# Kernel tuning notes

Hardware: AMD Instinct MI355X
Metric: run time of the kernel (lower is better)

The kernel has to match this reference:

```python
import jax, jax.numpy as jnp
import numpy as np

TEMPERATURE = 0.1
INF = 1e8
SIGMA = (5.0, 1.0)
LABEL_TYPE = ("cont", "cat")
CAT_SIM = (0.0, 0.5)
ALPHA = (1.0, 1.0)
N, D = 4096, 128


def _label_weights(y, label_type, sigma, cat_sim):
    # y: [2N] label values; returns row-normalized RBF weight matrix [2N, 2N]
    gamma = 1.0 / (2.0 * sigma ** 2)
    d2 = (y[:, None] - y[None, :]) ** 2
    w = jnp.exp(-gamma * d2)
    if label_type == "cat":
        # rbf == 1 exactly iff labels equal; others snapped to cat_similarity
        w = jnp.where(w == 1.0, 1.0, cat_sim)
    n2 = w.shape[0]
    w = w * (1.0 - jnp.eye(n2, dtype=w.dtype))
    w = w / jnp.sum(w, axis=1, keepdims=True)
    return w


def setup_inputs() -> dict:
    key = jax.random.key(0)
    k1, k2, k3, k4 = jax.random.split(key, 4)
    z_i = jax.random.normal(k1, (N, D), dtype=jnp.float32)
    z_j = jax.random.normal(k2, (N, D), dtype=jnp.float32)
    cont = jax.random.normal(k3, (N,), dtype=jnp.float32) * 10.0  # e.g. age
    cat = jax.random.randint(k4, (N,), 0, 3).astype(jnp.float32)   # e.g. class id
    labels = jnp.stack([cont, cat], axis=1)  # [N, 2]
    return {"z_i": z_i, "z_j": z_j, "labels": labels}


def reference(z_i, z_j, labels):
    n = z_i.shape[0]
    zi = z_i / jnp.linalg.norm(z_i, axis=-1, keepdims=True)
    zj = z_j / jnp.linalg.norm(z_j, axis=-1, keepdims=True)
    eye = INF * jnp.eye(n, dtype=zi.dtype)
    sim_zii = zi @ zi.T / TEMPERATURE - eye
    sim_zjj = zj @ zj.T / TEMPERATURE - eye
    sim_zij = zi @ zj.T / TEMPERATURE
    sim_Z = jnp.concatenate(
        [jnp.concatenate([sim_zii, sim_zij], axis=1),
         jnp.concatenate([sim_zij.T, sim_zjj], axis=1)], axis=0)  # [2N, 2N]
    log_sim_Z = jax.nn.log_softmax(sim_Z, axis=1)
    loss = jnp.zeros((), dtype=sim_Z.dtype)
    for i, (lt, s, cs, a) in enumerate(zip(LABEL_TYPE, SIGMA, CAT_SIM, ALPHA)):
        y = jnp.tile(labels[:, i], 2)  # [2N] == repeat(2,1).flatten()
        w = _label_weights(y, lt, s, cs)
        loss = loss + (-1.0 / n) * jnp.sum(w * log_sim_Z) * a
    return loss
```

## Files before the change

### kernel.cpp

```cpp
#include <hip/hip_runtime.h>
#include <hip/hip_bf16.h>
#include <math.h>

#define NP 4096
#define DD 128
#define N2 8192
#define TINV 10.0f
#define SHIFT 10.0f
#define C1 14.4269504f
#define NGL2 -0.0288539004f

typedef __attribute__((ext_vector_type(8))) short bf16x8;
typedef __attribute__((ext_vector_type(4))) float f32x4;
typedef __attribute__((ext_vector_type(4))) int i32x4;

__device__ __forceinline__ float bf2f(short s) {
  return __uint_as_float(((unsigned)(unsigned short)s) << 16);
}

#define GLDS(g, l)                                                                   \
  __builtin_amdgcn_global_load_lds((__attribute__((address_space(1))) const void*)(g), \
                                   (__attribute__((address_space(3))) void*)(l), 16, 0, 0)

__device__ __forceinline__ float dpp_red16(float x) {
  x += __int_as_float(__builtin_amdgcn_update_dpp(0, __float_as_int(x), 0x101, 0xF, 0xF, true));
  x += __int_as_float(__builtin_amdgcn_update_dpp(0, __float_as_int(x), 0x102, 0xF, 0xF, true));
  x += __int_as_float(__builtin_amdgcn_update_dpp(0, __float_as_int(x), 0x104, 0xF, 0xF, true));
  x += __int_as_float(__builtin_amdgcn_update_dpp(0, __float_as_int(x), 0x108, 0xF, 0xF, true));
  return x;
}

__global__ __launch_bounds__(256) void kprep(const float* __restrict__ zi,
                                             const float* __restrict__ zj,
                                             const float* __restrict__ labels,
                                             __hip_bfloat16* __restrict__ Z,
                                             float4* __restrict__ rowinfo,
                                             double* __restrict__ accd,
                                             unsigned int* __restrict__ cnt,
                                             float* __restrict__ zsc) {
  int w = threadIdx.x >> 6, lane = threadIdx.x & 63;
  if (blockIdx.x < 2048) {
    int a = blockIdx.x * 4 + w;
    const float* src = (a < NP) ? (zi + (size_t)a * DD) : (zj + (size_t)(a - NP) * DD);
    float2 v = *(const float2*)(src + lane * 2);
    float ss = v.x * v.x + v.y * v.y;
#pragma unroll
    for (int m = 1; m < 64; m <<= 1) ss += __shfl_xor(ss, m);
    float rn = rsqrtf(ss);
    __hip_bfloat162 o;
    o.x = __float2bfloat16(v.x * rn);
    o.y = __float2bfloat16(v.y * rn);
    *(__hip_bfloat162*)(Z + (size_t)a * DD + lane * 2) = o;
  } else {
    int a = blockIdx.x - 2048;
    if (a == 0) {
      if (threadIdx.x == 0) { *accd = 0.0; cnt[0] = 0u; }
      for (int q = threadIdx.x; q < 384; q += 256) zsc[q] = 0.f;
    }
    float ca = labels[a * 2 + 0], ga = labels[a * 2 + 1];
    float s1 = 0.f, c2 = 0.f;
    for (int m = threadIdx.x; m < NP; m += 256) {
      float2 lm = *(const float2*)(labels + m * 2);
      float dy = ca - lm.x;
      s1 += __builtin_amdgcn_exp2f(dy * dy * NGL2);
      c2 += (ga == lm.y) ? 1.f : 0.f;
    }
#pragma unroll
    for (int m = 1; m < 64; m <<= 1) {
      s1 += __shfl_xor(s1, m);
      c2 += __shfl_xor(c2, m);
    }
    __shared__ float sh[8];
    if (lane == 0) { sh[w] = s1; sh[4 + w] = c2; }
    __syncthreads();
    if (threadIdx.x == 0) {
      s1 = sh[0] + sh[1] + sh[2] + sh[3];
      c2 = sh[4] + sh[5] + sh[6] + sh[7];
      float rs1 = 2.f * s1 - 1.f;
      float rs2 = (float)NP + c2 - 1.f;
      float4 ri = make_float4(ca, TINV / rs1, ga, TINV / rs2);
      rowinfo[a] = ri;
      rowinfo[a + NP] = ri;
    }
  }
}

__global__ __launch_bounds__(512, 4) void kmain(const __hip_bfloat16* __restrict__ Zp,
                                                const float4* __restrict__ rowinfo,
                                                const float* __restrict__ labels,
                                                float2* __restrict__ part,
                                                float* __restrict__ zsc) {
  __shared__ char lds[2 * 128 * 256 + 4 * 512 * 4];

  int id = (blockIdx.x & 7) * 268 + (blockIdx.x >> 3);
  const int t = threadIdx.x;
  const int lane = t & 63, w = t >> 6;

  if (id >= 2080) {
    int b = id - 2080;
    int c = t & 127, rgrp = t >> 7;
    int r0 = b * 128 + rgrp * 32;
    float s0 = 0.f, s1 = 0.f, s2 = 0.f;
    for (int k = 0; k < 32; ++k) {
      int r = r0 + k;
      float zf = bf2f(((const short*)Zp)[(size_t)r * DD + c]);
      float g = labels[(r & (NP - 1)) * 2 + 1];
      s0 += (g == 0.f) ? zf : 0.f;
      s1 += (g == 1.f) ? zf : 0.f;
      s2 += (g == 2.f) ? zf : 0.f;
    }
    float* sh = (float*)lds;
    sh[(rgrp * 3 + 0) * 128 + c] = s0;
    sh[(rgrp * 3 + 1) * 128 + c] = s1;
    sh[(rgrp * 3 + 2) * 128 + c] = s2;
    __syncthreads();
    if (t < 384) {
      int cls = t >> 7, cc = t & 127;
      float v = sh[(0 * 3 + cls) * 128 + cc] + sh[(1 * 3 + cls) * 128 + cc] +
                sh[(2 * 3 + cls) * 128 + cc] + sh[(3 * 3 + cls) * 128 + cc];
      atomicAdd(&zsc[cls * 128 + cc], v);
    }
    return;
  }

  char* ldsA = lds;
  char* ldsB = lds + 128 * 256;
  float* lacc = (float*)(lds + 2 * 128 * 256);
  int tb = id;
  int I = (int)((129.0f - sqrtf(16641.0f - 8.0f * (float)tb)) * 0.5f);
  while (I * (129 - I) / 2 > tb) --I;
  while ((I + 1) * (128 - I) / 2 <= tb) ++I;
  int J = I + (tb - I * (129 - I) / 2);
  const bool diag = (I == J);
  const int row0 = I * 128, col0 = J * 128;
  const char* gZ = (const char*)Zp;
  const char* ldsBp = diag ? ldsA : ldsB;

  const int wr = w >> 2, wc = w & 3;
  const int lrow = lane & 15, lgrp = lane >> 4;

#pragma unroll
  for (int i = 0; i < 4; ++i) {
    int chunk = t + i * 512;
    int r = chunk >> 4;
    int bc = (chunk & 15) << 4;
    int srcc = bc ^ ((r & 7) << 4);
    int uoff = ((t & ~63) + i * 512) * 16;
    GLDS(gZ + (size_t)(row0 + r) * 256 + srcc, ldsA + uoff);
  }
  if (!diag) {
#pragma unroll
    for (int i = 0; i < 4; ++i) {
      int chunk = t + i * 512;
      int r = chunk >> 4;
      int bc = (chunk & 15) << 4;
      int srcc = bc ^ ((r & 7) << 4);
      int uoff = ((t & ~63) + i * 512) * 16;
      GLDS(gZ + (size_t)(col0 + r) * 256 + srcc, ldsB + uoff);
    }
  }
  __syncthreads();

  f32x4 acc[4][2] = {};
#pragma unroll
  for (int kk = 0; kk < 4; ++kk) {
    int bcol = kk * 64 + (lgrp << 4);
    bf16x8 af[4], bfv[2];
#pragma unroll
    for (int mi = 0; mi < 4; ++mi) {
      int r = wr * 64 + mi * 16 + lrow;
      af[mi] = *(const bf16x8*)(ldsA + r * 256 + (bcol ^ ((r & 7) << 4)));
    }
#pragma unroll
    for (int ni = 0; ni < 2; ++ni) {
      int r = wc * 32 + ni * 16 + lrow;
      bfv[ni] = *(const bf16x8*)(ldsBp + r * 256 + (bcol ^ ((r & 7) << 4)));
    }
#pragma unroll
    for (int mi = 0; mi < 4; ++mi)
#pragma unroll
      for (int ni = 0; ni < 2; ++ni)
        acc[mi][ni] = __builtin_amdgcn_mfma_f32_16x16x32_bf16(af[mi], bfv[ni], acc[mi][ni], 0, 0, 0);
  }

  float2 rbv[2];
#pragma unroll
  for (int ni = 0; ni < 2; ++ni)
    rbv[ni] = *(const float2*)&rowinfo[col0 + wc * 32 + ni * 16 + lrow];

  if (!diag) {
    float ec[2] = {0.f, 0.f}, pc[2] = {0.f, 0.f};
#pragma unroll
    for (int mi = 0; mi < 4; ++mi) {
      int a0 = row0 + wr * 64 + mi * 16 + lgrp * 4;
#pragma unroll
      for (int j = 0; j < 4; ++j) {
        float2 ri = *(const float2*)&rowinfo[a0 + j];
        float es = 0.f, pa = 0.f;
#pragma unroll
        for (int ni = 0; ni < 2; ++ni) {
          float v = acc[mi][ni][j];
          float e = __builtin_amdgcn_exp2f(fmaf(v, C1, -C1));
          float dy = ri.x - rbv[ni].x;
          float wu = __builtin_amdgcn_exp2f(dy * dy * NGL2);
          es += e;
          ec[ni] += e;
          pa = fmaf(wu, v, pa);
          pc[ni] = fmaf(wu, v, pc[ni]);
        }
        es = dpp_red16(es);
        float wsum = dpp_red16(pa * ri.y);
        if (lrow == 0) {
          int idx = wr * 64 + mi * 16 + lgrp * 4 + j;
          lacc[wc * 512 + 2 * idx] = es;
          lacc[wc * 512 + 2 * idx + 1] = wsum;
        }
      }
    }
#pragma unroll
    for (int ni = 0; ni < 2; ++ni) {
      float wcol = pc[ni] * rbv[ni].y;
      float e2 = ec[ni] + __shfl_xor(ec[ni], 16);
      e2 += __shfl_xor(e2, 32);
      float w2 = wcol + __shfl_xor(wcol, 16);
      w2 += __shfl_xor(w2, 32);
      if (lane < 16) {
        int idx = 128 + wc * 32 + ni * 16 + lane;
        lacc[wr * 512 + 2 * idx] = e2;
        lacc[wr * 512 + 2 * idx + 1] = w2;
      }
    }
  } else {
#pragma unroll
    for (int mi = 0; mi < 4; ++mi) {
      int a0 = row0 + wr * 64 + mi * 16 + lgrp * 4;
#pragma unroll
      for (int j = 0; j < 4; ++j) {
        int a = a0 + j;
        float2 ri = *(const float2*)&rowinfo[a0 + j];
        float es = 0.f, pa = 0.f;
#pragma unroll
        for (int ni = 0; ni < 2; ++ni) {
          float v = acc[mi][ni][j];
          float nd = (a != col0 + wc * 32 + ni * 16 + lrow) ? 1.f : 0.f;
          float e = __builtin_amdgcn_exp2f(fmaf(v, C1, -C1)) * nd;
          float dy = ri.x - rbv[ni].x;
          float wu = __builtin_amdgcn_exp2f(dy * dy * NGL2) * nd;
          es += e;
          pa = fmaf(wu, v, pa);
        }
        es = dpp_red16(es);
        float wsum = dpp_red16(pa * ri.y);
        if (lrow == 0) {
          int idx = wr * 64 + mi * 16 + lgrp * 4 + j;
          lacc[wc * 512 + 2 * idx] = es;
          lacc[wc * 512 + 2 * idx + 1] = wsum;
        }
      }
    }
    if (w < 2 && lane < 32) {
#pragma unroll
      for (int i = 0; i < 8; ++i) lacc[w * 512 + 256 + lane * 8 + i] = 0.f;
    }
  }

  __syncthreads();
  if (t < 256) {
    float2 p0 = ((float2*)lacc)[t];
    float2 p1 = ((float2*)lacc)[256 + t];
    float2 o;
    if (t < 128) {
      float2 p2 = ((float2*)lacc)[512 + t];
      float2 p3 = ((float2*)lacc)[768 + t];
      o.x = (p0.x + p1.x) + (p2.x + p3.x);
      o.y = (p0.y + p1.y) + (p2.y + p3.y);
    } else {
      o.x = p0.x + p1.x;
      o.y = p0.y + p1.y;
    }
    part[(size_t)tb * 256 + t] = o;
  }
}

__global__ __launch_bounds__(512) void kreduce(const float2* __restrict__ part,
                                               const __hip_bfloat16* __restrict__ Z,
                                               const float4* __restrict__ rowinfo,
                                               const float* __restrict__ zsc,
                                               double* __restrict__ accd,
                                               unsigned int* __restrict__ cnt,
                                               float* __restrict__ out) {
  int T = blockIdx.x;
  int t = threadIdx.x;
  int r = t & 127, q = t >> 7;
  float es = 0.f, ws = 0.f;
  int tb0 = T * (129 - T) / 2;
  for (int k = q; k < 64 - T; k += 4) {
    float2 v = part[(size_t)(tb0 + k) * 256 + r];
    es += v.x;
    ws += v.y;
  }
  for (int I = q; I < T; I += 4) {
    float2 v = part[(size_t)(I * (129 - I) / 2 + T - I) * 256 + 128 + r];
    es += v.x;
    ws += v.y;
  }
  __shared__ float sess[512], swss[512];
  sess[q * 128 + r] = es;
  swss[q * 128 + r] = ws;
  __syncthreads();

  double val = 0.0;
  if (t < 128) {
    es = sess[t] + sess[128 + t] + sess[256 + t] + sess[384 + t];
    ws = swss[t] + swss[128 + t] + swss[256 + t] + swss[384 + t];
    int a = T * 128 + t;
    float4 ri = rowinfo[a];
    int cls = (int)ri.z;
    const float* zc = zsc + cls * DD;
    float d1 = 0.f, d2 = 0.f;
    const __hip_bfloat16* zrow = Z + (size_t)a * DD;
#pragma unroll
    for (int k = 0; k < 16; ++k) {
      bf16x8 zv = *(const bf16x8*)(zrow + k * 8);
#pragma unroll
      for (int e = 0; e < 8; ++e) {
        int col = k * 8 + e;
        float zf = bf2f(zv[e]);
        float tot = zsc[col] + zsc[128 + col] + zsc[256 + col];
        d1 = fmaf(zf, tot, d1);
        d2 = fmaf(zf, zc[col], d2);
      }
    }
    ws += (0.5f * (d1 - 1.0f) + 0.5f * (d2 - 1.0f)) * ri.w;
    val = (double)ws - 2.0 * (double)(SHIFT + __logf(es));
  }
#pragma unroll
  for (int m = 1; m < 64; m <<= 1) val += __shfl_xor(val, m);
  __shared__ double shd[8];
  if ((t & 63) == 0) shd[t >> 6] = val;
  __syncthreads();
  if (t == 0) {
    double bsum = shd[0] + shd[1] + shd[2] + shd[3] + shd[4] + shd[5] + shd[6] + shd[7];
    atomicAdd(accd, bsum);
    __threadfence();
    unsigned int old = atomicAdd(cnt, 1u);
    if (old == 63u) {
      double tot = atomicAdd(accd, 0.0);
      out[0] = (float)(-tot / (double)NP);
    }
  }
}

extern "C" void kernel_launch(void* const* d_in, const int* in_sizes, int n_in,
                              void* d_out, int out_size, void* d_ws, size_t ws_size,
                              hipStream_t stream) {
  const float* zi = (const float*)d_in[0];
  const float* zj = (const float*)d_in[1];
  const float* labels = (const float*)d_in[2];
  float* out = (float*)d_out;
  char* ws = (char*)d_ws;

  float4* rowinfo = (float4*)ws;
  double* accd = (double*)(ws + 128 * 1024);
  unsigned int* cnt = (unsigned int*)(ws + 128 * 1024 + 8);
  float* zsc = (float*)(ws + 132 * 1024);
  __hip_bfloat16* Z = (__hip_bfloat16*)(ws + 256 * 1024);
  float2* part = (float2*)(ws + 256 * 1024 + 2 * 1024 * 1024);

  kprep<<<6144, 256, 0, stream>>>(zi, zj, labels, Z, rowinfo, accd, cnt, zsc);
  kmain<<<2144, 512, 0, stream>>>(Z, rowinfo, labels, part, zsc);
  kreduce<<<64, 512, 0, stream>>>(part, Z, rowinfo, zsc, accd, cnt, out);
}
```

Baseline: 59.09 us.

## Make kmain persistent and prefetch the next tile during the epilogue

Replaces the 2144-block grid with 512 persistent blocks. Each block walks a strided list of tile IDs, and the zsc class-sum work is folded into the same loop. After the MFMA loop and a barrier, the next tile's global-to-LDS loads are issued before the exp/weight epilogue runs, so load latency overlaps the epilogue. This reduces block launch and first-load stalls, but the persistent blocks may load-balance less evenly and rely on barriers to order the LDS DMA.

Measured after the change: 87.73 us. 48.5% more time.

```diff
diff --git a/kernel.cpp b/kernel.cpp
--- a/kernel.cpp
+++ b/kernel.cpp
@@ -91,64 +91,27 @@
                                                 float2* __restrict__ part,
                                                 float* __restrict__ zsc) {
   __shared__ char lds[2 * 128 * 256 + 4 * 512 * 4];
-
-  int id = (blockIdx.x & 7) * 268 + (blockIdx.x >> 3);
-  const int t = threadIdx.x;
-  const int lane = t & 63, w = t >> 6;
-
-  if (id >= 2080) {
-    int b = id - 2080;
-    int c = t & 127, rgrp = t >> 7;
-    int r0 = b * 128 + rgrp * 32;
-    float s0 = 0.f, s1 = 0.f, s2 = 0.f;
-    for (int k = 0; k < 32; ++k) {
-      int r = r0 + k;
-      float zf = bf2f(((const short*)Zp)[(size_t)r * DD + c]);
-      float g = labels[(r & (NP - 1)) * 2 + 1];
-      s0 += (g == 0.f) ? zf : 0.f;
-      s1 += (g == 1.f) ? zf : 0.f;
-      s2 += (g == 2.f) ? zf : 0.f;
-    }
-    float* sh = (float*)lds;
-    sh[(rgrp * 3 + 0) * 128 + c] = s0;
-    sh[(rgrp * 3 + 1) * 128 + c] = s1;
-    sh[(rgrp * 3 + 2) * 128 + c] = s2;
-    __syncthreads();
-    if (t < 384) {
-      int cls = t >> 7, cc = t & 127;
-      float v = sh[(0 * 3 + cls) * 128 + cc] + sh[(1 * 3 + cls) * 128 + cc] +
-                sh[(2 * 3 + cls) * 128 + cc] + sh[(3 * 3 + cls) * 128 + cc];
-      atomicAdd(&zsc[cls * 128 + cc], v);
-    }
-    return;
-  }
-
   char* ldsA = lds;
   char* ldsB = lds + 128 * 256;
   float* lacc = (float*)(lds + 2 * 128 * 256);
-  int tb = id;
-  int I = (int)((129.0f - sqrtf(16641.0f - 8.0f * (float)tb)) * 0.5f);
-  while (I * (129 - I) / 2 > tb) --I;
-  while ((I + 1) * (128 - I) / 2 <= tb) ++I;
-  int J = I + (tb - I * (129 - I) / 2);
-  const bool diag = (I == J);
-  const int row0 = I * 128, col0 = J * 128;
-  const char* gZ = (const char*)Zp;
-  const char* ldsBp = diag ? ldsA : ldsB;
-
+
+  const int t = threadIdx.x;
+  const int lane = t & 63, w = t >> 6;
   const int wr = w >> 2, wc = w & 3;
   const int lrow = lane & 15, lgrp = lane >> 4;
-
-#pragma unroll
-  for (int i = 0; i < 4; ++i) {
-    int chunk = t + i * 512;
-    int r = chunk >> 4;
-    int bc = (chunk & 15) << 4;
-    int srcc = bc ^ ((r & 7) << 4);
-    int uoff = ((t & ~63) + i * 512) * 16;
-    GLDS(gZ + (size_t)(row0 + r) * 256 + srcc, ldsA + uoff);
-  }
-  if (!diag) {
+  const char* gZ = (const char*)Zp;
+
+  const int x = blockIdx.x & 7, l = blockIdx.x >> 3;
+  const int idbase = x * 268, idend = idbase + 268;
+
+  auto decode = [](int tb, int& I, int& J) {
+    int i0 = (int)((129.0f - sqrtf(16641.0f - 8.0f * (float)tb)) * 0.5f);
+    while (i0 * (129 - i0) / 2 > tb) --i0;
+    while ((i0 + 1) * (128 - i0) / 2 <= tb) ++i0;
+    I = i0;
+    J = i0 + (tb - i0 * (129 - i0) / 2);
+  };
+  auto stage = [&](int row0, int col0, bool diag) {
 #pragma unroll
     for (int i = 0; i < 4; ++i) {
       int chunk = t + i * 512;
@@ -156,129 +119,199 @@
       int bc = (chunk & 15) << 4;
       int srcc = bc ^ ((r & 7) << 4);
       int uoff = ((t & ~63) + i * 512) * 16;
-      GLDS(gZ + (size_t)(col0 + r) * 256 + srcc, ldsB + uoff);
+      GLDS(gZ + (size_t)(row0 + r) * 256 + srcc, ldsA + uoff);
+    }
+    if (!diag) {
+#pragma unroll
+      for (int i = 0; i < 4; ++i) {
+        int chunk = t + i * 512;
+        int r = chunk >> 4;
+        int bc = (chunk & 15) << 4;
+        int srcc = bc ^ ((r & 7) << 4);
+        int uoff = ((t & ~63) + i * 512) * 16;
+        GLDS(gZ + (size_t)(col0 + r) * 256 + srcc, ldsB + uoff);
+      }
+    }
+  };
+
+  int curI = 0, curJ = 0;
+  {
+    int id0 = idbase + l;
+    if (id0 < 2080) {
+      decode(id0, curI, curJ);
+      stage(curI * 128, curJ * 128, curI == curJ);
     }
   }
   __syncthreads();
 
-  f32x4 acc[4][2] = {};
-#pragma unroll
-  for (int kk = 0; kk < 4; ++kk) {
-    int bcol = kk * 64 + (lgrp << 4);
-    bf16x8 af[4], bfv[2];
-#pragma unroll
-    for (int mi = 0; mi < 4; ++mi) {
-      int r = wr * 64 + mi * 16 + lrow;
-      af[mi] = *(const bf16x8*)(ldsA + r * 256 + (bcol ^ ((r & 7) << 4)));
-    }
-#pragma unroll
-    for (int ni = 0; ni < 2; ++ni) {
-      int r = wc * 32 + ni * 16 + lrow;
-      bfv[ni] = *(const bf16x8*)(ldsBp + r * 256 + (bcol ^ ((r & 7) << 4)));
-    }
-#pragma unroll
-    for (int mi = 0; mi < 4; ++mi)
-#pragma unroll
-      for (int ni = 0; ni < 2; ++ni)
-        acc[mi][ni] = __builtin_amdgcn_mfma_f32_16x16x32_bf16(af[mi], bfv[ni], acc[mi][ni], 0, 0, 0);
-  }
-
-  float2 rbv[2];
-#pragma unroll
-  for (int ni = 0; ni < 2; ++ni)
-    rbv[ni] = *(const float2*)&rowinfo[col0 + wc * 32 + ni * 16 + lrow];
-
-  if (!diag) {
-    float ec[2] = {0.f, 0.f}, pc[2] = {0.f, 0.f};
-#pragma unroll
-    for (int mi = 0; mi < 4; ++mi) {
-      int a0 = row0 + wr * 64 + mi * 16 + lgrp * 4;
-#pragma unroll
-      for (int j = 0; j < 4; ++j) {
-        float2 ri = *(const float2*)&rowinfo[a0 + j];
-        float es = 0.f, pa = 0.f;
-#pragma unroll
-        for (int ni = 0; ni < 2; ++ni) {
-          float v = acc[mi][ni][j];
-          float e = __builtin_amdgcn_exp2f(fmaf(v, C1, -C1));
-          float dy = ri.x - rbv[ni].x;
-          float wu = __builtin_amdgcn_exp2f(dy * dy * NGL2);
-          es += e;
-          ec[ni] += e;
-          pa = fmaf(wu, v, pa);
-          pc[ni] = fmaf(wu, v, pc[ni]);
+  for (int k = 0; ; ++k) {
+    int id = idbase + l + 64 * k;
+    if (id >= idend) break;
+
+    if (id >= 2080) {
+      __syncthreads();
+      int b = id - 2080;
+      int c = t & 127, rgrp = t >> 7;
+      int r0 = b * 128 + rgrp * 32;
+      float s0 = 0.f, s1 = 0.f, s2 = 0.f;
+      for (int kk = 0; kk < 32; ++kk) {
+        int r = r0 + kk;
+        float zf = bf2f(((const short*)Zp)[(size_t)r * DD + c]);
+        float g = labels[(r & (NP - 1)) * 2 + 1];
+        s0 += (g == 0.f) ? zf : 0.f;
+        s1 += (g == 1.f) ? zf : 0.f;
+        s2 += (g == 2.f) ? zf : 0.f;
+      }
+      float* sh = (float*)lds;
+      sh[(rgrp * 3 + 0) * 128 + c] = s0;
+      sh[(rgrp * 3 + 1) * 128 + c] = s1;
+      sh[(rgrp * 3 + 2) * 128 + c] = s2;
+      __syncthreads();
+      if (t < 384) {
+        int cls = t >> 7, cc = t & 127;
+        float v = sh[(0 * 3 + cls) * 128 + cc] + sh[(1 * 3 + cls) * 128 + cc] +
+                  sh[(2 * 3 + cls) * 128 + cc] + sh[(3 * 3 + cls) * 128 + cc];
+        atomicAdd(&zsc[cls * 128 + cc], v);
+      }
+      continue;
+    }
+
+    const int row0 = curI * 128, col0 = curJ * 128;
+    const bool diag = (curI == curJ);
+    const char* ldsBp = diag ? ldsA : ldsB;
+
+    f32x4 acc[4][2] = {};
+#pragma unroll
+    for (int kk = 0; kk < 4; ++kk) {
+      int bcol = kk * 64 + (lgrp << 4);
+      bf16x8 af[4], bfv[2];
+#pragma unroll
+      for (int mi = 0; mi < 4; ++mi) {
+        int r = wr * 64 + mi * 16 + lrow;
+        af[mi] = *(const bf16x8*)(ldsA + r * 256 + (bcol ^ ((r & 7) << 4)));
+      }
+#pragma unroll
+      for (int ni = 0; ni < 2; ++ni) {
+        int r = wc * 32 + ni * 16 + lrow;
+        bfv[ni] = *(const bf16x8*)(ldsBp + r * 256 + (bcol ^ ((r & 7) << 4)));
+      }
+#pragma unroll
+      for (int mi = 0; mi < 4; ++mi)
+#pragma unroll
+        for (int ni = 0; ni < 2; ++ni)
+          acc[mi][ni] = __builtin_amdgcn_mfma_f32_16x16x32_bf16(af[mi], bfv[ni], acc[mi][ni], 0, 0, 0);
+    }
+
+    __syncthreads();
+
+    int idn = id + 64;
+    int nI = curI, nJ = curJ;
+    if (idn < idend && idn < 2080) {
+      decode(idn, nI, nJ);
+      stage(nI * 128, nJ * 128, nI == nJ);
+    }
+
+    float2 rbv[2];
+#pragma unroll
+    for (int ni = 0; ni < 2; ++ni)
+      rbv[ni] = *(const float2*)&rowinfo[col0 + wc * 32 + ni * 16 + lrow];
+
+    if (!diag) {
+      float ec[2] = {0.f, 0.f}, pc[2] = {0.f, 0.f};
+#pragma unroll
+      for (int mi = 0; mi < 4; ++mi) {
+        int a0 = row0 + wr * 64 + mi * 16 + lgrp * 4;
+#pragma unroll
+        for (int j = 0; j < 4; ++j) {
+          float2 ri = *(const float2*)&rowinfo[a0 + j];
+          float es = 0.f, pa = 0.f;
+#pragma unroll
+          for (int ni = 0; ni < 2; ++ni) {
+            float v = acc[mi][ni][j];
+            float e = __builtin_amdgcn_exp2f(fmaf(v, C1, -C1));
+            float dy = ri.x - rbv[ni].x;
+            float wu = __builtin_amdgcn_exp2f(dy * dy * NGL2);
+            es += e;
+            ec[ni] += e;
+            pa = fmaf(wu, v, pa);
+            pc[ni] = fmaf(wu, v, pc[ni]);
+          }
+          es = dpp_red16(es);
+          float wsum = dpp_red16(pa * ri.y);
+          if (lrow == 0) {
+            int idx = wr * 64 + mi * 16 + lgrp * 4 + j;
+            lacc[wc * 512 + 2 * idx] = es;
+            lacc[wc * 512 + 2 * idx + 1] = wsum;
+          }
         }
-        es = dpp_red16(es);
-        float wsum = dpp_red16(pa * ri.y);
-        if (lrow == 0) {
-          int idx = wr * 64 + mi * 16 + lgrp * 4 + j;
-          lacc[wc * 512 + 2 * idx] = es;
-          lacc[wc * 512 + 2 * idx + 1] = wsum;
+      }
+#pragma unroll
+      for (int ni = 0; ni < 2; ++ni) {
+        float wcol = pc[ni] * rbv[ni].y;
+        float e2 = ec[ni] + __shfl_xor(ec[ni], 16);
+        e2 += __shfl_xor(e2, 32);
+        float w2 = wcol + __shfl_xor(wcol, 16);
+        w2 += __shfl_xor(w2, 32);
+        if (lane < 16) {
+          int idx = 128 + wc * 32 + ni * 16 + lane;
+          lacc[wr * 512 + 2 * idx] = e2;
+          lacc[wr * 512 + 2 * idx + 1] = w2;
         }
       }
-    }
-#pragma unroll
-    for (int ni = 0; ni < 2; ++ni) {
-      float wcol = pc[ni] * rbv[ni].y;
-      float e2 = ec[ni] + __shfl_xor(ec[ni], 16);
-      e2 += __shfl_xor(e2, 32);
-      float w2 = wcol + __shfl_xor(wcol, 16);
-      w2 += __shfl_xor(w2, 32);
-      if (lane < 16) {
-        int idx = 128 + wc * 32 + ni * 16 + lane;
-        lacc[wr * 512 + 2 * idx] = e2;
-        lacc[wr * 512 + 2 * idx + 1] = w2;
-      }
-    }
-  } else {
-#pragma unroll
-    for (int mi = 0; mi < 4; ++mi) {
-      int a0 = row0 + wr * 64 + mi * 16 + lgrp * 4;
-#pragma unroll
-      for (int j = 0; j < 4; ++j) {
-        int a = a0 + j;
-        float2 ri = *(const float2*)&rowinfo[a0 + j];
-        float es = 0.f, pa = 0.f;
-#pragma unroll
-        for (int ni = 0; ni < 2; ++ni) {
-          float v = acc[mi][ni][j];
-          float nd = (a != col0 + wc * 32 + ni * 16 + lrow) ? 1.f : 0.f;
-          float e = __builtin_amdgcn_exp2f(fmaf(v, C1, -C1)) * nd;
-          float dy = ri.x - rbv[ni].x;
-          float wu = __builtin_amdgcn_exp2f(dy * dy * NGL2) * nd;
-          es += e;
-          pa = fmaf(wu, v, pa);
+    } else {
+#pragma unroll
+      for (int mi = 0; mi < 4; ++mi) {
+        int a0 = row0 + wr * 64 + mi * 16 + lgrp * 4;
+#pragma unroll
+        for (int j = 0; j < 4; ++j) {
+          int a = a0 + j;
+          float2 ri = *(const float2*)&rowinfo[a0 + j];
+          float es = 0.f, pa = 0.f;
+#pragma unroll
+          for (int ni = 0; ni < 2; ++ni) {
+            float v = acc[mi][ni][j];
+            float nd = (a != col0 + wc * 32 + ni * 16 + lrow) ? 1.f : 0.f;
+            float e = __builtin_amdgcn_exp2f(fmaf(v, C1, -C1)) * nd;
+            float dy = ri.x - rbv[ni].x;
+            float wu = __builtin_amdgcn_exp2f(dy * dy * NGL2) * nd;
+            es += e;
+            pa = fmaf(wu, v, pa);
+          }
+          es = dpp_red16(es);
+          float wsum = dpp_red16(pa * ri.y);
+          if (lrow == 0) {
+            int idx = wr * 64 + mi * 16 + lgrp * 4 + j;
+            lacc[wc * 512 + 2 * idx] = es;
+            lacc[wc * 512 + 2 * idx + 1] = wsum;
+          }
         }
-        es = dpp_red16(es);
-        float wsum = dpp_red16(pa * ri.y);
-        if (lrow == 0) {
-          int idx = wr * 64 + mi * 16 + lgrp * 4 + j;
-          lacc[wc * 512 + 2 * idx] = es;
-          lacc[wc * 512 + 2 * idx + 1] = wsum;
-        }
-      }
-    }
-    if (w < 2 && lane < 32) {
-#pragma unroll
-      for (int i = 0; i < 8; ++i) lacc[w * 512 + 256 + lane * 8 + i] = 0.f;
-    }
-  }
-
-  __syncthreads();
-  if (t < 256) {
-    float2 p0 = ((float2*)lacc)[t];
-    float2 p1 = ((float2*)lacc)[256 + t];
-    float2 o;
-    if (t < 128) {
-      float2 p2 = ((float2*)lacc)[512 + t];
-      float2 p3 = ((float2*)lacc)[768 + t];
-      o.x = (p0.x + p1.x) + (p2.x + p3.x);
-      o.y = (p0.y + p1.y) + (p2.y + p3.y);
-    } else {
-      o.x = p0.x + p1.x;
-      o.y = p0.y + p1.y;
-    }
-    part[(size_t)tb * 256 + t] = o;
+      }
+      if (w < 2 && lane < 32) {
+#pragma unroll
+        for (int i = 0; i < 8; ++i) lacc[w * 512 + 256 + lane * 8 + i] = 0.f;
+      }
+    }
+
+    __syncthreads();
+
+    if (t < 256) {
+      float2 p0 = ((float2*)lacc)[t];
+      float2 p1 = ((float2*)lacc)[256 + t];
+      float2 o;
+      if (t < 128) {
+        float2 p2 = ((float2*)lacc)[512 + t];
+        float2 p3 = ((float2*)lacc)[768 + t];
+        o.x = (p0.x + p1.x) + (p2.x + p3.x);
+        o.y = (p0.y + p1.y) + (p2.y + p3.y);
+      } else {
+        o.x = p0.x + p1.x;
+        o.y = p0.y + p1.y;
+      }
+      part[(size_t)id * 256 + t] = o;
+    }
+
+    curI = nI;
+    curJ = nJ;
   }
 }
 
@@ -368,6 +401,6 @@
   float2* part = (float2*)(ws + 256 * 1024 + 2 * 1024 * 1024);
 
   kprep<<<6144, 256, 0, stream>>>(zi, zj, labels, Z, rowinfo, accd, cnt, zsc);
-  kmain<<<2144, 512, 0, stream>>>(Z, rowinfo, labels, part, zsc);
+  kmain<<<512, 512, 0, stream>>>(Z, rowinfo, labels, part, zsc);
   kreduce<<<64, 512, 0, stream>>>(part, Z, rowinfo, zsc, accd, cnt, out);
 }
```
